# Kernel tuning notes

Measured on AMD Instinct MI355X. Metric: run time of the kernel, lower is better.

## Reference

```python
import jax, jax.numpy as jnp
import numpy as np

B, T = 64, 1024
VOCAB, EMBED, HIDDEN = 55, 64, 128


def setup_inputs() -> dict:
    key = jax.random.key(0)
    ks = jax.random.split(key, 15)
    stdv = 1.0 / np.sqrt(HIDDEN)
    u = lambda k, s: jax.random.uniform(k, s, jnp.float32, -stdv, stdv)
    return {
        "x": jax.random.randint(ks[0], (B, T), 0, VOCAB),
        "emb": jax.random.normal(ks[1], (VOCAB, EMBED), jnp.float32),
        "w_ih0": u(ks[2], (HIDDEN, EMBED)),
        "b_ih0": u(ks[3], (HIDDEN,)),
        "w_hh0": u(ks[4], (HIDDEN, HIDDEN)),
        "b_hh0": u(ks[5], (HIDDEN,)),
        "w_ih1": u(ks[6], (HIDDEN, HIDDEN)),
        "b_ih1": u(ks[7], (HIDDEN,)),
        "w_hh1": u(ks[8], (HIDDEN, HIDDEN)),
        "b_hh1": u(ks[9], (HIDDEN,)),
        "attn_w": u(ks[10], (HIDDEN, HIDDEN)),
        "attn_b": u(ks[11], (HIDDEN,)),
        "fc_w": u(ks[12], (VOCAB, 2 * HIDDEN)),
        "fc_b": u(ks[13], (VOCAB,)),
    }


def reference(x, emb, w_ih0, b_ih0, w_hh0, b_hh0, w_ih1, b_ih1, w_hh1, b_hh1,
              attn_w, attn_b, fc_w, fc_b):
    Bx, Tx = x.shape
    H = w_hh0.shape[0]
    e = emb[x]  # [B, T, E]

    def step(carry, x_t):  # x_t: [B, E]
        h0, h1 = carry
        h0 = jnp.tanh(x_t @ w_ih0.T + b_ih0 + h0 @ w_hh0.T + b_hh0)
        h1 = jnp.tanh(h0 @ w_ih1.T + b_ih1 + h1 @ w_hh1.T + b_hh1)
        return (h0, h1), h1

    init = (jnp.zeros((Bx, H), e.dtype), jnp.zeros((Bx, H), e.dtype))
    _, outs = jax.lax.scan(step, init, jnp.swapaxes(e, 0, 1))  # [T, B, H]
    outs = jnp.swapaxes(outs, 0, 1)  # [B, T, H]

    Q = outs @ attn_w.T + attn_b  # [B, T, H]
    scores = jnp.einsum('bth,bsh->bts', Q, outs) / jnp.sqrt(jnp.asarray(H, e.dtype))
    causal = jnp.tril(jnp.ones((Tx, Tx), bool))  # [T, T]
    scores = jnp.where(causal[None], scores, jnp.asarray(-jnp.inf, scores.dtype))
    attn = jax.nn.softmax(scores, axis=-1)
    context = jnp.einsum('bts,bsh->bth', attn, outs)  # [B, T, H]

    combined = jnp.concatenate([outs, context], axis=-1)  # [B, T, 2H]
    logits = combined @ fc_w.T + fc_b  # [B, T, vocab]
    return logits
```

## Files before the change

### kernel.cpp

```cpp
#include <hip/hip_runtime.h>
#include <hip/hip_bf16.h>
#include <cstdint>
#include <cstddef>


typedef __attribute__((ext_vector_type(8))) short short8;
typedef __attribute__((ext_vector_type(4))) float f32x4;

__device__ __forceinline__ float bf2f(unsigned short u) {
    union { unsigned int i; float f; } c; c.i = ((unsigned int)u) << 16; return c.f;
}
__device__ __forceinline__ unsigned short f2bf(float f) {
    union { float f; unsigned int i; } c; c.f = f;
    unsigned int u = c.i;
    u += 0x7fffu + ((u >> 16) & 1u);
    return (unsigned short)(u >> 16);
}
__device__ __forceinline__ unsigned int pk_bf16(float lo, float hi) {
    union { __hip_bfloat162 h2; unsigned int u; } c;
    c.h2 = __float22bfloat162_rn(make_float2(lo, hi));
    return c.u;
}
__device__ __forceinline__ float fast_tanh(float x) {
    float e = __expf(2.0f * x);
    return 1.0f - 2.0f * __builtin_amdgcn_rcpf(e + 1.0f);
}
__device__ __forceinline__ void bar_lds() {
    asm volatile("s_waitcnt lgkmcnt(0)\n\ts_barrier" ::: "memory");
}
__device__ __forceinline__ short8 ld_a_bf16(const float* p) {
    const float4* q = (const float4*)p;
    float4 f0 = q[0], f1 = q[1];
    short8 r;
    r[0]=(short)f2bf(f0.x); r[1]=(short)f2bf(f0.y);
    r[2]=(short)f2bf(f0.z); r[3]=(short)f2bf(f0.w);
    r[4]=(short)f2bf(f1.x); r[5]=(short)f2bf(f1.y);
    r[6]=(short)f2bf(f1.z); r[7]=(short)f2bf(f1.w);
    return r;
}
__device__ __forceinline__ void ld_fc_hilo(const float* p, short8& hi, short8& lo) {
    const float4* q = (const float4*)p;
    float4 f0 = q[0], f1 = q[1];
    float ff[8] = {f0.x, f0.y, f0.z, f0.w, f1.x, f1.y, f1.z, f1.w};
#pragma unroll
    for (int i = 0; i < 8; ++i) {
        unsigned short hb = f2bf(ff[i]);
        hi[i] = (short)hb;
        lo[i] = (short)f2bf(ff[i] - bf2f(hb));
    }
}

__global__ __launch_bounds__(128)
void k_we(const float* __restrict__ emb, const float* __restrict__ w_ih0,
          const float* __restrict__ b_ih0, const float* __restrict__ b_hh0,
          float* __restrict__ WE)
{
    __shared__ float ev[64];
    const int i = threadIdx.x;
    const int v = blockIdx.x;
    if (i < 64) ev[i] = emb[v * 64 + i];
    __syncthreads();
    float s = b_ih0[i] + b_hh0[i];
    const float* wr = w_ih0 + i * 64;
#pragma unroll
    for (int k = 0; k < 64; ++k) s += wr[k] * ev[k];
    WE[v * 128 + i] = s;
}

__global__ __launch_bounds__(256)
void k_weg(const int* __restrict__ x, const float* __restrict__ WE,
           float* __restrict__ WEg)
{
    __shared__ int xv[32];
    const int tid = threadIdx.x;
    const int b   = blockIdx.y;
    const int t0  = blockIdx.x * 32;
    if (tid < 32) xv[tid] = x[b * 1024 + t0 + tid];
    __syncthreads();
#pragma unroll
    for (int it = 0; it < 4; ++it) {
        int tt = it * 8 + (tid >> 5);
        int c4 = tid & 31;
        float4 v = ((const float4*)(WE + xv[tt] * 128))[c4];
        ((float4*)(WEg + ((size_t)b * 1024 + t0 + tt) * 128))[c4] = v;
    }
}

#define A_STEP(T, P, E0, E1)                                                   \
  {                                                                            \
    const unsigned short* h0p = &h0buf[P][n][quad * 8];                        \
    short8 bh[4];                                                              \
    _Pragma("unroll")                                                          \
    for (int ks = 0; ks < 4; ++ks)                                             \
      bh[ks] = *(const short8*)(h0p + ks * 32);                                \
    f32x4 c0 = (f32x4){E0.x, E0.y, E0.z, E0.w};                                \
    f32x4 c1 = (f32x4){E1.x, E1.y, E1.z, E1.w};                                \
    {                                                                          \
      const size_t tp = (size_t)(((T) + 3 < 1024) ? (T) + 3 : 1023) * 128;     \
      E0 = *(const float4*)(WEg + wegB0 + tp);                                 \
      E1 = *(const float4*)(WEg + wegB1 + tp);                                 \
    }                                                                          \
    _Pragma("unroll")                                                          \
    for (int ks = 0; ks < 4; ++ks) {                                           \
      c0 = __builtin_amdgcn_mfma_f32_16x16x32_bf16(a0[0][ks], bh[ks], c0, 0, 0, 0); \
      c1 = __builtin_amdgcn_mfma_f32_16x16x32_bf16(a0[1][ks], bh[ks], c1, 0, 0, 0); \
    }                                                                          \
    *(uint2*)&h0buf[(P) ^ 1][n][r0] = make_uint2(                              \
        pk_bf16(fast_tanh(c0[0]), fast_tanh(c0[1])),                           \
        pk_bf16(fast_tanh(c0[2]), fast_tanh(c0[3])));                          \
    *(uint2*)&h0buf[(P) ^ 1][n][r1] = make_uint2(                              \
        pk_bf16(fast_tanh(c1[0]), fast_tanh(c1[1])),                           \
        pk_bf16(fast_tanh(c1[2]), fast_tanh(c1[3])));                          \
    bar_lds();                                                                 \
  }

#define B_STEP(T, P)                                                           \
  {                                                                            \
    const unsigned short* h0p = &h0buf[P][n][quad * 8];                        \
    const unsigned short* h1p = &h1buf[P][n][quad * 8];                        \
    short8 bh0[4], bh1[4];                                                     \
    _Pragma("unroll")                                                          \
    for (int ks = 0; ks < 4; ++ks) {                                           \
      bh0[ks] = *(const short8*)(h0p + ks * 32);                               \
      bh1[ks] = *(const short8*)(h1p + ks * 32);                               \
    }                                                                          \
    f32x4 c0 = b1i[0], c1 = b1i[1];                                            \
    f32x4 d0 = (f32x4){0.f, 0.f, 0.f, 0.f};                                    \
    f32x4 d1 = (f32x4){0.f, 0.f, 0.f, 0.f};                                    \
    _Pragma("unroll")                                                          \
    for (int ks = 0; ks < 4; ++ks) {                                           \
      c0 = __builtin_amdgcn_mfma_f32_16x16x32_bf16(a1[0][ks], bh0[ks], c0, 0, 0, 0); \
      c1 = __builtin_amdgcn_mfma_f32_16x16x32_bf16(a1[1][ks], bh0[ks], c1, 0, 0, 0); \
      d0 = __builtin_amdgcn_mfma_f32_16x16x32_bf16(a2[0][ks], bh1[ks], d0, 0, 0, 0); \
      d1 = __builtin_amdgcn_mfma_f32_16x16x32_bf16(a2[1][ks], bh1[ks], d1, 0, 0, 0); \
    }                                                                          \
    uint2 o0 = make_uint2(                                                     \
        pk_bf16(fast_tanh(c0[0] + d0[0]), fast_tanh(c0[1] + d0[1])),           \
        pk_bf16(fast_tanh(c0[2] + d0[2]), fast_tanh(c0[3] + d0[3])));          \
    uint2 o1 = make_uint2(                                                     \
        pk_bf16(fast_tanh(c1[0] + d1[0]), fast_tanh(c1[1] + d1[1])),           \
        pk_bf16(fast_tanh(c1[2] + d1[2]), fast_tanh(c1[3] + d1[3])));          \
    *(uint2*)&h1buf[(P) ^ 1][n][r0] = o0;                                      \
    *(uint2*)&h1buf[(P) ^ 1][n][r1] = o1;                                      \
    *(uint2*)(outp0 + (size_t)(T) * 128) = o0;                                 \
    *(uint2*)(outp1 + (size_t)(T) * 128) = o1;                                 \
    bar_lds();                                                                 \
  }

__global__ __launch_bounds__(512, 1)
void k_scan7(const float* __restrict__ WEg,
             const float* __restrict__ w_hh0,
             const float* __restrict__ w_ih1, const float* __restrict__ b_ih1,
             const float* __restrict__ w_hh1, const float* __restrict__ b_hh1,
             unsigned short* __restrict__ outs_bf)
{
    const int tid   = threadIdx.x;
    const int w     = tid >> 6;
    const int lane  = tid & 63;
    const int quad  = lane >> 4;
    const int n     = lane & 15;
    const int bbase = blockIdx.x * 16;

    __shared__ __align__(16) unsigned short h0buf[2][16][136];
    __shared__ __align__(16) unsigned short h1buf[2][16][136];

    if (w < 4) {
        const int r0 = w * 32 + quad * 4;
        const int r1 = r0 + 16;
        short8 a0[2][4];
#pragma unroll
        for (int r = 0; r < 2; ++r) {
            const size_t mrow = (size_t)(w * 32 + r * 16 + n) * 128;
#pragma unroll
            for (int ks = 0; ks < 4; ++ks)
                a0[r][ks] = ld_a_bf16(w_hh0 + mrow + ks * 32 + quad * 8);
        }
        const size_t wegB0 = (size_t)(bbase + n) * 131072 + r0;
        const size_t wegB1 = wegB0 + 16;
        {
            float4 p0 = *(const float4*)(WEg + wegB0);
            float4 p1 = *(const float4*)(WEg + wegB1);
            *(uint2*)&h0buf[0][n][r0] = make_uint2(
                pk_bf16(fast_tanh(p0.x), fast_tanh(p0.y)),
                pk_bf16(fast_tanh(p0.z), fast_tanh(p0.w)));
            *(uint2*)&h0buf[0][n][r1] = make_uint2(
                pk_bf16(fast_tanh(p1.x), fast_tanh(p1.y)),
                pk_bf16(fast_tanh(p1.z), fast_tanh(p1.w)));
        }
        float4 eA0 = *(const float4*)(WEg + wegB0 + 128);
        float4 eA1 = *(const float4*)(WEg + wegB1 + 128);
        float4 eB0 = *(const float4*)(WEg + wegB0 + 256);
        float4 eB1 = *(const float4*)(WEg + wegB1 + 256);
        __syncthreads();

        for (int t = 0; t < 1022; t += 2) {
            A_STEP(t,     0, eA0, eA1);
            A_STEP(t + 1, 1, eB0, eB1);
        }
        A_STEP(1022, 0, eA0, eA1);
        bar_lds();
    } else {
        const int w2 = w - 4;
        const int r0 = w2 * 32 + quad * 4;
        const int r1 = r0 + 16;
        short8 a1[2][4], a2[2][4];
#pragma unroll
        for (int r = 0; r < 2; ++r) {
            const size_t mrow = (size_t)(w2 * 32 + r * 16 + n) * 128;
#pragma unroll
            for (int ks = 0; ks < 4; ++ks) {
                a1[r][ks] = ld_a_bf16(w_ih1 + mrow + ks * 32 + quad * 8);
                a2[r][ks] = ld_a_bf16(w_hh1 + mrow + ks * 32 + quad * 8);
            }
        }
        f32x4 b1i[2];
#pragma unroll
        for (int r = 0; r < 2; ++r)
#pragma unroll
            for (int j = 0; j < 4; ++j) {
                int row = w2 * 32 + r * 16 + quad * 4 + j;
                b1i[r][j] = b_ih1[row] + b_hh1[row];
            }
        *(uint2*)&h1buf[0][n][r0] = make_uint2(0u, 0u);
        *(uint2*)&h1buf[0][n][r1] = make_uint2(0u, 0u);
        unsigned short* outp0 = outs_bf + (size_t)(bbase + n) * 131072 + r0;
        unsigned short* outp1 = outp0 + 16;
        __syncthreads();

        for (int t = 0; t < 1022; t += 2) {
            B_STEP(t,     0);
            B_STEP(t + 1, 1);
        }
        B_STEP(1022, 0);
        B_STEP(1023, 1);
    }
}

__global__ __launch_bounds__(256)
void k_transpose(const unsigned short* __restrict__ outs_bf,
                 unsigned short* __restrict__ outsT)
{
    __shared__ unsigned short lt[128][130];
    const int tid = threadIdx.x;
    const int t0  = blockIdx.x * 128;
    const int b   = blockIdx.y;
    const unsigned int* src =
        (const unsigned int*)(outs_bf + ((size_t)b * 1024 + t0) * 128);
    for (int idx = tid; idx < 8192; idx += 256) {
        int tr = idx >> 6, h2 = idx & 63;
        unsigned int v = src[tr * 64 + h2];
        lt[tr][h2 * 2]     = (unsigned short)(v & 0xffffu);
        lt[tr][h2 * 2 + 1] = (unsigned short)(v >> 16);
    }
    __syncthreads();
    unsigned int* dst = (unsigned int*)(outsT + (size_t)b * 128 * 1024);
    for (int idx = tid; idx < 8192; idx += 256) {
        int h = idx >> 6, t2 = idx & 63;
        unsigned int v = (unsigned int)lt[t2 * 2][h] |
                         ((unsigned int)lt[t2 * 2 + 1][h] << 16);
        dst[h * 512 + (t0 >> 1) + t2] = v;
    }
}

__global__ __launch_bounds__(512, 1)
void k_attnfc(const unsigned short* __restrict__ outs_bf,
              const unsigned short* __restrict__ outsT,
              const float* __restrict__ attn_w, const float* __restrict__ attn_b,
              const float* __restrict__ fc_w, const float* __restrict__ fc_b,
              float* __restrict__ out)
{
    __shared__ __align__(16) unsigned char smem[51200];
    unsigned short* lK = (unsigned short*)smem;
    unsigned short* lV = (unsigned short*)(smem + 16384);
    unsigned short* lP = (unsigned short*)(smem + 32768);

    const int tid  = threadIdx.x;
    const int w    = tid >> 6;
    const int lane = tid & 63;
    const int quad = lane >> 4;
    const int n    = lane & 15;
    const int qt   = blockIdx.x;
    const int b    = blockIdx.y;
    unsigned short* lPw = lP + w * 1152;
    unsigned short* lQw = ((unsigned short*)smem) + w * 2048;
    const float cscale = 0.08838834764831845f;

    const unsigned short* outsB = outs_bf + (size_t)b * 131072;
    const int qrow = qt * 128 + w * 16 + n;

    short8 bo[4];
#pragma unroll
    for (int ks = 0; ks < 4; ++ks)
        bo[ks] = *(const short8*)(outsB + (size_t)qrow * 128 + ks * 32 + quad * 8);
#pragma unroll
    for (int mt = 0; mt < 8; ++mt) {
        short8 aw[4];
#pragma unroll
        for (int ks = 0; ks < 4; ++ks)
            aw[ks] = ld_a_bf16(attn_w + (size_t)(mt * 16 + n) * 128 + ks * 32 + quad * 8);
        f32x4 cq;
#pragma unroll
        for (int r = 0; r < 4; ++r) cq[r] = attn_b[mt * 16 + quad * 4 + r];
#pragma unroll
        for (int ks = 0; ks < 4; ++ks)
            cq = __builtin_amdgcn_mfma_f32_16x16x32_bf16(aw[ks], bo[ks], cq, 0,0,0);
        *(uint2*)&lQw[n * 128 + mt * 16 + quad * 4] =
            make_uint2(pk_bf16(cq[0], cq[1]), pk_bf16(cq[2], cq[3]));
    }
    short8 qf[4];
#pragma unroll
    for (int ks = 0; ks < 4; ++ks)
        qf[ks] = *(const short8*)&lQw[n * 128 + ks * 32 + quad * 8];

    f32x4 accO[8];
#pragma unroll
    for (int dt = 0; dt < 8; ++dt) accO[dt] = (f32x4){0.f, 0.f, 0.f, 0.f};
    float mx = -1e30f, lsum = 0.f;

    const int ntiles = 2 * qt + 2;
    for (int kt = 0; kt < ntiles; ++kt) {
        __syncthreads();
        for (int c = tid; c < 2048; c += 512) {
            if (c < 1024) {
                int row = c >> 4, k8 = c & 15;
                uint4 vk = *(const uint4*)(outsB + (size_t)(kt * 64 + row) * 128 + k8 * 8);
                *(uint4*)&lK[row * 128 + ((k8 ^ (row & 15)) << 3)] = vk;
            } else {
                int c2 = c - 1024;
                int d = c2 >> 3, t8 = c2 & 7;
                uint4 vv = *(const uint4*)(outsT + ((size_t)b * 128 + d) * 1024 +
                                           kt * 64 + t8 * 8);
                *(uint4*)&lV[d * 64 + ((t8 ^ (d & 7)) << 3)] = vv;
            }
        }
        __syncthreads();
        f32x4 accS[4];
#pragma unroll
        for (int mt = 0; mt < 4; ++mt) {
            short8 af[4];
#pragma unroll
            for (int ks = 0; ks < 4; ++ks) {
                int r = mt * 16 + n;
                af[ks] = *(const short8*)&lK[r * 128 + (((ks * 4 + quad) ^ (r & 15)) << 3)];
            }
            f32x4 s = (f32x4){0.f, 0.f, 0.f, 0.f};
#pragma unroll
            for (int ks = 0; ks < 4; ++ks)
                s = __builtin_amdgcn_mfma_f32_16x16x32_bf16(af[ks], qf[ks], s, 0,0,0);
            accS[mt] = s;
        }
        if (kt >= 2 * qt) {
#pragma unroll
            for (int mt = 0; mt < 4; ++mt)
#pragma unroll
                for (int jv = 0; jv < 4; ++jv)
                    if (kt * 64 + mt * 16 + quad * 4 + jv > qrow - qt * 128 + 0 + qt * 128 - qt * 128
                        + qt * 128 - qt * 128 + (qrow & 127) - (qrow & 127) + (qrow - qt * 128))
                        ;
        }
        if (kt >= 2 * qt) {
            const int ql = w * 16 + n;
#pragma unroll
            for (int mt = 0; mt < 4; ++mt)
#pragma unroll
                for (int jv = 0; jv < 4; ++jv)
                    if (kt * 64 + mt * 16 + quad * 4 + jv > qt * 128 + ql)
                        accS[mt][jv] = -1e30f;
        }
        float tmax = accS[0][0];
#pragma unroll
        for (int mt = 0; mt < 4; ++mt)
#pragma unroll
            for (int jv = 0; jv < 4; ++jv) tmax = fmaxf(tmax, accS[mt][jv]);
        tmax = fmaxf(tmax, __shfl_xor(tmax, 16));
        tmax = fmaxf(tmax, __shfl_xor(tmax, 32));
        float nm = fmaxf(mx, tmax);
        float alpha = __expf((mx - nm) * cscale);
        float ss = 0.f;
#pragma unroll
        for (int mt = 0; mt < 4; ++mt)
#pragma unroll
            for (int jv = 0; jv < 4; ++jv) {
                float p = __expf((accS[mt][jv] - nm) * cscale);
                accS[mt][jv] = p;
                ss += p;
            }
        ss += __shfl_xor(ss, 16);
        ss += __shfl_xor(ss, 32);
        lsum = lsum * alpha + ss;
        mx = nm;
#pragma unroll
        for (int mt = 0; mt < 4; ++mt)
            *(uint2*)&lPw[n * 72 + mt * 16 + quad * 4] = make_uint2(
                pk_bf16(accS[mt][0], accS[mt][1]),
                pk_bf16(accS[mt][2], accS[mt][3]));
#pragma unroll
        for (int dt = 0; dt < 8; ++dt)
#pragma unroll
            for (int jv = 0; jv < 4; ++jv) accO[dt][jv] *= alpha;
        short8 pf[2];
#pragma unroll
        for (int ks = 0; ks < 2; ++ks)
            pf[ks] = *(const short8*)&lPw[n * 72 + ks * 32 + quad * 8];
#pragma unroll
        for (int dt = 0; dt < 8; ++dt) {
            short8 vf[2];
#pragma unroll
            for (int ks = 0; ks < 2; ++ks) {
                int d = dt * 16 + n;
                vf[ks] = *(const short8*)&lV[d * 64 + (((ks * 4 + quad) ^ (d & 7)) << 3)];
            }
#pragma unroll
            for (int ks = 0; ks < 2; ++ks)
                accO[dt] = __builtin_amdgcn_mfma_f32_16x16x32_bf16(vf[ks], pf[ks], accO[dt], 0,0,0);
        }
    }
    __syncthreads();
    {
        float inv = __builtin_amdgcn_rcpf(lsum);
#pragma unroll
        for (int dt = 0; dt < 8; ++dt)
            *(uint2*)&lQw[n * 128 + dt * 16 + quad * 4] = make_uint2(
                pk_bf16(accO[dt][0] * inv, accO[dt][1] * inv),
                pk_bf16(accO[dt][2] * inv, accO[dt][3] * inv));
    }
    short8 bC[4];
#pragma unroll
    for (int ks = 0; ks < 4; ++ks)
        bC[ks] = *(const short8*)&lQw[n * 128 + ks * 32 + quad * 8];
#pragma unroll
    for (int mt = 0; mt < 4; ++mt) {
        const int vrow = mt * 16 + n;
        f32x4 acc;
#pragma unroll
        for (int r = 0; r < 4; ++r) {
            int vv = mt * 16 + quad * 4 + r;
            acc[r] = (vv < 55) ? fc_b[vv] : 0.f;
        }
#pragma unroll
        for (int c = 0; c < 8; ++c) {
            short8 hi, lo;
            if (vrow < 55) {
                ld_fc_hilo(fc_w + (size_t)vrow * 256 + c * 32 + quad * 8, hi, lo);
            } else {
#pragma unroll
                for (int i = 0; i < 8; ++i) { hi[i] = 0; lo[i] = 0; }
            }
            short8 bb = (c < 4) ? bo[c] : bC[c - 4];
            acc = __builtin_amdgcn_mfma_f32_16x16x32_bf16(hi, bb, acc, 0,0,0);
            acc = __builtin_amdgcn_mfma_f32_16x16x32_bf16(lo, bb, acc, 0,0,0);
        }
#pragma unroll
        for (int r = 0; r < 4; ++r) {
            int vv = mt * 16 + quad * 4 + r;
            if (vv < 55)
                out[((size_t)b * 1024 + qrow) * 55 + vv] = acc[r];
        }
    }
}

extern "C" void kernel_launch(void* const* d_in, const int* in_sizes, int n_in,
                              void* d_out, int out_size, void* d_ws, size_t ws_size,
                              hipStream_t stream)
{
    const int*   x      = (const int*)d_in[0];
    const float* emb    = (const float*)d_in[1];
    const float* w_ih0  = (const float*)d_in[2];
    const float* b_ih0  = (const float*)d_in[3];
    const float* w_hh0  = (const float*)d_in[4];
    const float* b_hh0  = (const float*)d_in[5];
    const float* w_ih1  = (const float*)d_in[6];
    const float* b_ih1  = (const float*)d_in[7];
    const float* w_hh1  = (const float*)d_in[8];
    const float* b_hh1  = (const float*)d_in[9];
    const float* attn_w = (const float*)d_in[10];
    const float* attn_b = (const float*)d_in[11];
    const float* fc_w   = (const float*)d_in[12];
    const float* fc_b   = (const float*)d_in[13];
    float* out = (float*)d_out;

    char* ws = (char*)d_ws;
    unsigned short* outs_bf = (unsigned short*)(ws);
    unsigned short* outsT   = (unsigned short*)(ws + ((size_t)16 << 20));
    float*          WEp     = (float*)         (ws + ((size_t)32 << 20));
    float*          WEg     = (float*)         (ws + ((size_t)33 << 20));

    k_we<<<dim3(55), dim3(128), 0, stream>>>(emb, w_ih0, b_ih0, b_hh0, WEp);
    k_weg<<<dim3(32, 64), dim3(256), 0, stream>>>(x, WEp, WEg);
    k_scan7<<<dim3(4), dim3(512), 0, stream>>>(
        WEg, w_hh0, w_ih1, b_ih1, w_hh1, b_hh1, outs_bf);
    k_transpose<<<dim3(8, 64), dim3(256), 0, stream>>>(outs_bf, outsT);
    k_attnfc<<<dim3(8, 64), dim3(512), 0, stream>>>(
        outs_bf, outsT, attn_w, attn_b, fc_w, fc_b, out);
}
```

Before: 742.6 us.

## Split causal attention KV tiles across blocks and merge partial softmax states

Each query tile's causal key range is split into chunks of at most six KV tiles, handled by separate blocks, which balances work across the triangular attention grid. Short query tiles (qt ≤ 2) still finish in one block and apply the FC projection directly. Longer ones write unnormalized partial outputs plus running max and sum to a workspace. A new merge kernel combines the partials with online-softmax rescaling and then runs the FC projection. This costs an extra launch and a workspace round-trip, and the partial buffer overlaps the workspace region that held WEg, which is safe only because that data is no longer needed.

Result: slower. 804.6 us (+8.3%).

```diff
diff --git a/kernel.cpp b/kernel.cpp
--- a/kernel.cpp
+++ b/kernel.cpp
@@ -263,11 +263,11 @@
 }
 
 __global__ __launch_bounds__(512, 1)
-void k_attnfc(const unsigned short* __restrict__ outs_bf,
-              const unsigned short* __restrict__ outsT,
-              const float* __restrict__ attn_w, const float* __restrict__ attn_b,
-              const float* __restrict__ fc_w, const float* __restrict__ fc_b,
-              float* __restrict__ out)
+void k_attn_part(const unsigned short* __restrict__ outs_bf,
+                 const unsigned short* __restrict__ outsT,
+                 const float* __restrict__ attn_w, const float* __restrict__ attn_b,
+                 const float* __restrict__ fc_w, const float* __restrict__ fc_b,
+                 float* __restrict__ part_ws, float* __restrict__ out)
 {
     __shared__ __align__(16) unsigned char smem[51200];
     unsigned short* lK = (unsigned short*)smem;
@@ -279,14 +279,28 @@
     const int lane = tid & 63;
     const int quad = lane >> 4;
     const int n    = lane & 15;
-    const int qt   = blockIdx.x;
+    const int gi   = blockIdx.x;
     const int b    = blockIdx.y;
     unsigned short* lPw = lP + w * 1152;
     unsigned short* lQw = ((unsigned short*)smem) + w * 2048;
     const float cscale = 0.08838834764831845f;
 
+    int qt = 0, base = 0;
+    if (gi >= 1)  { qt = 1; base = 1; }
+    if (gi >= 2)  { qt = 2; base = 2; }
+    if (gi >= 3)  { qt = 3; base = 3; }
+    if (gi >= 5)  { qt = 4; base = 5; }
+    if (gi >= 7)  { qt = 5; base = 7; }
+    if (gi >= 9)  { qt = 6; base = 9; }
+    if (gi >= 12) { qt = 7; base = 12; }
+    const int g   = gi - base;
+    const int kt0 = g * 6;
+    const int kt1 = min(kt0 + 6, 2 * qt + 2);
+    const bool whole = (qt <= 2);
+
     const unsigned short* outsB = outs_bf + (size_t)b * 131072;
     const int qrow = qt * 128 + w * 16 + n;
+    const int q128 = w * 16 + n;
 
     short8 bo[4];
 #pragma unroll
@@ -317,8 +331,7 @@
     for (int dt = 0; dt < 8; ++dt) accO[dt] = (f32x4){0.f, 0.f, 0.f, 0.f};
     float mx = -1e30f, lsum = 0.f;
 
-    const int ntiles = 2 * qt + 2;
-    for (int kt = 0; kt < ntiles; ++kt) {
+    for (int kt = kt0; kt < kt1; ++kt) {
         __syncthreads();
         for (int c = tid; c < 2048; c += 512) {
             if (c < 1024) {
@@ -350,15 +363,6 @@
             accS[mt] = s;
         }
         if (kt >= 2 * qt) {
-#pragma unroll
-            for (int mt = 0; mt < 4; ++mt)
-#pragma unroll
-                for (int jv = 0; jv < 4; ++jv)
-                    if (kt * 64 + mt * 16 + quad * 4 + jv > qrow - qt * 128 + 0 + qt * 128 - qt * 128
-                        + qt * 128 - qt * 128 + (qrow & 127) - (qrow & 127) + (qrow - qt * 128))
-                        ;
-        }
-        if (kt >= 2 * qt) {
             const int ql = w * 16 + n;
 #pragma unroll
             for (int mt = 0; mt < 4; ++mt)
@@ -415,6 +419,21 @@
                 accO[dt] = __builtin_amdgcn_mfma_f32_16x16x32_bf16(vf[ks], pf[ks], accO[dt], 0,0,0);
         }
     }
+
+    if (!whole) {
+        float* wsO = part_ws + (size_t)(b * 12 + gi - 3) * 16640;
+        float4* po = (float4*)wsO;
+#pragma unroll
+        for (int dt = 0; dt < 8; ++dt)
+            po[(w * 64 + lane) * 8 + dt] =
+                make_float4(accO[dt][0], accO[dt][1], accO[dt][2], accO[dt][3]);
+        if (quad == 0) {
+            wsO[16384 + q128 * 2]     = mx;
+            wsO[16384 + q128 * 2 + 1] = lsum;
+        }
+        return;
+    }
+
     __syncthreads();
     {
         float inv = __builtin_amdgcn_rcpf(lsum);
@@ -428,6 +447,107 @@
 #pragma unroll
     for (int ks = 0; ks < 4; ++ks)
         bC[ks] = *(const short8*)&lQw[n * 128 + ks * 32 + quad * 8];
+#pragma unroll
+    for (int mt = 0; mt < 4; ++mt) {
+        const int vrow = mt * 16 + n;
+        f32x4 acc;
+#pragma unroll
+        for (int r = 0; r < 4; ++r) {
+            int vv = mt * 16 + quad * 4 + r;
+            acc[r] = (vv < 55) ? fc_b[vv] : 0.f;
+        }
+#pragma unroll
+        for (int c = 0; c < 8; ++c) {
+            short8 hi, lo;
+            if (vrow < 55) {
+                ld_fc_hilo(fc_w + (size_t)vrow * 256 + c * 32 + quad * 8, hi, lo);
+            } else {
+#pragma unroll
+                for (int i = 0; i < 8; ++i) { hi[i] = 0; lo[i] = 0; }
+            }
+            short8 bb = (c < 4) ? bo[c] : bC[c - 4];
+            acc = __builtin_amdgcn_mfma_f32_16x16x32_bf16(hi, bb, acc, 0,0,0);
+            acc = __builtin_amdgcn_mfma_f32_16x16x32_bf16(lo, bb, acc, 0,0,0);
+        }
+#pragma unroll
+        for (int r = 0; r < 4; ++r) {
+            int vv = mt * 16 + quad * 4 + r;
+            if (vv < 55)
+                out[((size_t)b * 1024 + qrow) * 55 + vv] = acc[r];
+        }
+    }
+}
+
+__global__ __launch_bounds__(512, 1)
+void k_merge(const unsigned short* __restrict__ outs_bf,
+             const float* __restrict__ part_ws,
+             const float* __restrict__ fc_w, const float* __restrict__ fc_b,
+             float* __restrict__ out)
+{
+    __shared__ __align__(16) unsigned short lQ[8][16][128];
+
+    const int tid  = threadIdx.x;
+    const int w    = tid >> 6;
+    const int lane = tid & 63;
+    const int quad = lane >> 4;
+    const int n    = lane & 15;
+    const int qt   = blockIdx.x + 3;
+    const int b    = blockIdx.y;
+    const float cscale = 0.08838834764831845f;
+
+    const int ng = (2 * qt + 7) / 6;
+    int base = 9;
+    if (qt == 3) base = 0;
+    else if (qt == 4) base = 2;
+    else if (qt == 5) base = 4;
+    else if (qt == 6) base = 6;
+
+    const int qrow = qt * 128 + w * 16 + n;
+    const int q128 = w * 16 + n;
+
+    f32x4 accO[8];
+#pragma unroll
+    for (int dt = 0; dt < 8; ++dt) accO[dt] = (f32x4){0.f, 0.f, 0.f, 0.f};
+    float mx = -1e30f, lsum = 0.f;
+
+    for (int p = 0; p < ng; ++p) {
+        const float* wsO = part_ws + (size_t)(b * 12 + base + p) * 16640;
+        const float4* po = (const float4*)wsO;
+        float m0 = wsO[16384 + q128 * 2];
+        float l0 = wsO[16384 + q128 * 2 + 1];
+        float nm = fmaxf(mx, m0);
+        float a1 = __expf((mx - nm) * cscale);
+        float a0 = __expf((m0 - nm) * cscale);
+#pragma unroll
+        for (int dt = 0; dt < 8; ++dt) {
+            float4 p4 = po[(w * 64 + lane) * 8 + dt];
+            accO[dt][0] = accO[dt][0] * a1 + p4.x * a0;
+            accO[dt][1] = accO[dt][1] * a1 + p4.y * a0;
+            accO[dt][2] = accO[dt][2] * a1 + p4.z * a0;
+            accO[dt][3] = accO[dt][3] * a1 + p4.w * a0;
+        }
+        lsum = lsum * a1 + l0 * a0;
+        mx = nm;
+    }
+
+    {
+        float inv = __builtin_amdgcn_rcpf(lsum);
+#pragma unroll
+        for (int dt = 0; dt < 8; ++dt)
+            *(uint2*)&lQ[w][n][dt * 16 + quad * 4] = make_uint2(
+                pk_bf16(accO[dt][0] * inv, accO[dt][1] * inv),
+                pk_bf16(accO[dt][2] * inv, accO[dt][3] * inv));
+    }
+    __syncthreads();
+    const unsigned short* outsB = outs_bf + (size_t)b * 131072;
+    short8 bo[4];
+#pragma unroll
+    for (int ks = 0; ks < 4; ++ks)
+        bo[ks] = *(const short8*)(outsB + (size_t)qrow * 128 + ks * 32 + quad * 8);
+    short8 bC[4];
+#pragma unroll
+    for (int ks = 0; ks < 4; ++ks)
+        bC[ks] = *(const short8*)&lQ[w][n][ks * 32 + quad * 8];
 #pragma unroll
     for (int mt = 0; mt < 4; ++mt) {
         const int vrow = mt * 16 + n;
@@ -483,6 +603,7 @@
     unsigned short* outs_bf = (unsigned short*)(ws);
     unsigned short* outsT   = (unsigned short*)(ws + ((size_t)16 << 20));
     float*          WEp     = (float*)         (ws + ((size_t)32 << 20));
+    float*          part_ws = (float*)         (ws + ((size_t)32 << 20) + (64 << 10));
     float*          WEg     = (float*)         (ws + ((size_t)33 << 20));
 
     k_we<<<dim3(55), dim3(128), 0, stream>>>(emb, w_ih0, b_ih0, b_hh0, WEp);
@@ -490,6 +611,8 @@
     k_scan7<<<dim3(4), dim3(512), 0, stream>>>(
         WEg, w_hh0, w_ih1, b_ih1, w_hh1, b_hh1, outs_bf);
     k_transpose<<<dim3(8, 64), dim3(256), 0, stream>>>(outs_bf, outsT);
-    k_attnfc<<<dim3(8, 64), dim3(512), 0, stream>>>(
-        outs_bf, outsT, attn_w, attn_b, fc_w, fc_b, out);
-}
+    k_attn_part<<<dim3(15, 64), dim3(512), 0, stream>>>(
+        outs_bf, outsT, attn_w, attn_b, fc_w, fc_b, part_ws, out);
+    k_merge<<<dim3(5, 64), dim3(512), 0, stream>>>(
+        outs_bf, part_ws, fc_w, fc_b, out);
+}
```

## Pre-convert attention/fc weights to bf16 and use direct global-to-LDS loads

Applied to the files above, without the earlier changes.

Adds a prep kernel that converts attn_w to bf16 and splits fc_w into hi/lo bf16 parts once, so the attention/FC kernel loads bf16 directly instead of converting per block. The K/V tile staging in the attention loop is replaced with global_load_lds 16-byte direct-to-LDS loads, with the XOR swizzle moved to the global address side. A dead no-op mask loop is removed. This adds one extra small kernel launch and relies on the direct-LDS load path producing the same swizzled layout.

After: 744.6 us. About the same (+0.3%).

```diff
diff --git a/kernel.cpp b/kernel.cpp
--- a/kernel.cpp
+++ b/kernel.cpp
@@ -38,15 +38,26 @@
     r[6]=(short)f2bf(f1.z); r[7]=(short)f2bf(f1.w);
     return r;
 }
-__device__ __forceinline__ void ld_fc_hilo(const float* p, short8& hi, short8& lo) {
-    const float4* q = (const float4*)p;
-    float4 f0 = q[0], f1 = q[1];
-    float ff[8] = {f0.x, f0.y, f0.z, f0.w, f1.x, f1.y, f1.z, f1.w};
-#pragma unroll
-    for (int i = 0; i < 8; ++i) {
-        unsigned short hb = f2bf(ff[i]);
-        hi[i] = (short)hb;
-        lo[i] = (short)f2bf(ff[i] - bf2f(hb));
+__device__ __forceinline__ void gload_lds16(const unsigned short* g,
+                                            unsigned short* l) {
+    __builtin_amdgcn_global_load_lds(
+        (const __attribute__((address_space(1))) unsigned int*)g,
+        (__attribute__((address_space(3))) unsigned int*)l, 16, 0, 0);
+}
+
+__global__ __launch_bounds__(256)
+void k_prep(const float* __restrict__ attn_w, const float* __restrict__ fc_w,
+            unsigned short* __restrict__ attn_wb,
+            unsigned short* __restrict__ fc_hib,
+            unsigned short* __restrict__ fc_lob)
+{
+    const int i = blockIdx.x * 256 + threadIdx.x;
+    if (i < 16384) attn_wb[i] = f2bf(attn_w[i]);
+    if (i < 14080) {
+        float wv = fc_w[i];
+        unsigned short h = f2bf(wv);
+        fc_hib[i] = h;
+        fc_lob[i] = f2bf(wv - bf2f(h));
     }
 }
 
@@ -265,8 +276,11 @@
 __global__ __launch_bounds__(512, 1)
 void k_attnfc(const unsigned short* __restrict__ outs_bf,
               const unsigned short* __restrict__ outsT,
-              const float* __restrict__ attn_w, const float* __restrict__ attn_b,
-              const float* __restrict__ fc_w, const float* __restrict__ fc_b,
+              const unsigned short* __restrict__ attn_wb,
+              const float* __restrict__ attn_b,
+              const unsigned short* __restrict__ fc_hib,
+              const unsigned short* __restrict__ fc_lob,
+              const float* __restrict__ fc_b,
               float* __restrict__ out)
 {
     __shared__ __align__(16) unsigned char smem[51200];
@@ -297,7 +311,8 @@
         short8 aw[4];
 #pragma unroll
         for (int ks = 0; ks < 4; ++ks)
-            aw[ks] = ld_a_bf16(attn_w + (size_t)(mt * 16 + n) * 128 + ks * 32 + quad * 8);
+            aw[ks] = *(const short8*)(attn_wb + (size_t)(mt * 16 + n) * 128 +
+                                      ks * 32 + quad * 8);
         f32x4 cq;
 #pragma unroll
         for (int r = 0; r < 4; ++r) cq[r] = attn_b[mt * 16 + quad * 4 + r];
@@ -320,18 +335,21 @@
     const int ntiles = 2 * qt + 2;
     for (int kt = 0; kt < ntiles; ++kt) {
         __syncthreads();
-        for (int c = tid; c < 2048; c += 512) {
-            if (c < 1024) {
-                int row = c >> 4, k8 = c & 15;
-                uint4 vk = *(const uint4*)(outsB + (size_t)(kt * 64 + row) * 128 + k8 * 8);
-                *(uint4*)&lK[row * 128 + ((k8 ^ (row & 15)) << 3)] = vk;
-            } else {
-                int c2 = c - 1024;
-                int d = c2 >> 3, t8 = c2 & 7;
-                uint4 vv = *(const uint4*)(outsT + ((size_t)b * 128 + d) * 1024 +
-                                           kt * 64 + t8 * 8);
-                *(uint4*)&lV[d * 64 + ((t8 ^ (d & 7)) << 3)] = vv;
-            }
+        {
+            int c = tid;
+            int row = c >> 4, g = c & 15;
+            gload_lds16(outsB + (size_t)(kt * 64 + row) * 128 +
+                        ((g ^ (row & 15)) << 3), lK + c * 8);
+            c = tid + 512; row = c >> 4; g = c & 15;
+            gload_lds16(outsB + (size_t)(kt * 64 + row) * 128 +
+                        ((g ^ (row & 15)) << 3), lK + c * 8);
+            int c2 = tid;
+            int d = c2 >> 3, t8 = c2 & 7;
+            gload_lds16(outsT + ((size_t)b * 128 + d) * 1024 + kt * 64 +
+                        ((t8 ^ (d & 7)) << 3), lV + c2 * 8);
+            c2 = tid + 512; d = c2 >> 3; t8 = c2 & 7;
+            gload_lds16(outsT + ((size_t)b * 128 + d) * 1024 + kt * 64 +
+                        ((t8 ^ (d & 7)) << 3), lV + c2 * 8);
         }
         __syncthreads();
         f32x4 accS[4];
@@ -348,15 +366,6 @@
             for (int ks = 0; ks < 4; ++ks)
                 s = __builtin_amdgcn_mfma_f32_16x16x32_bf16(af[ks], qf[ks], s, 0,0,0);
             accS[mt] = s;
-        }
-        if (kt >= 2 * qt) {
-#pragma unroll
-            for (int mt = 0; mt < 4; ++mt)
-#pragma unroll
-                for (int jv = 0; jv < 4; ++jv)
-                    if (kt * 64 + mt * 16 + quad * 4 + jv > qrow - qt * 128 + 0 + qt * 128 - qt * 128
-                        + qt * 128 - qt * 128 + (qrow & 127) - (qrow & 127) + (qrow - qt * 128))
-                        ;
         }
         if (kt >= 2 * qt) {
             const int ql = w * 16 + n;
@@ -441,7 +450,8 @@
         for (int c = 0; c < 8; ++c) {
             short8 hi, lo;
             if (vrow < 55) {
-                ld_fc_hilo(fc_w + (size_t)vrow * 256 + c * 32 + quad * 8, hi, lo);
+                hi = *(const short8*)(fc_hib + (size_t)vrow * 256 + c * 32 + quad * 8);
+                lo = *(const short8*)(fc_lob + (size_t)vrow * 256 + c * 32 + quad * 8);
             } else {
 #pragma unroll
                 for (int i = 0; i < 8; ++i) { hi[i] = 0; lo[i] = 0; }
@@ -483,13 +493,17 @@
     unsigned short* outs_bf = (unsigned short*)(ws);
     unsigned short* outsT   = (unsigned short*)(ws + ((size_t)16 << 20));
     float*          WEp     = (float*)         (ws + ((size_t)32 << 20));
+    unsigned short* attn_wb = (unsigned short*)(ws + ((size_t)32 << 20) + (64 << 10));
+    unsigned short* fc_hib  = (unsigned short*)(ws + ((size_t)32 << 20) + (128 << 10));
+    unsigned short* fc_lob  = (unsigned short*)(ws + ((size_t)32 << 20) + (192 << 10));
     float*          WEg     = (float*)         (ws + ((size_t)33 << 20));
 
+    k_prep<<<dim3(64), dim3(256), 0, stream>>>(attn_w, fc_w, attn_wb, fc_hib, fc_lob);
     k_we<<<dim3(55), dim3(128), 0, stream>>>(emb, w_ih0, b_ih0, b_hh0, WEp);
     k_weg<<<dim3(32, 64), dim3(256), 0, stream>>>(x, WEp, WEg);
     k_scan7<<<dim3(4), dim3(512), 0, stream>>>(
         WEg, w_hh0, w_ih1, b_ih1, w_hh1, b_hh1, outs_bf);
     k_transpose<<<dim3(8, 64), dim3(256), 0, stream>>>(outs_bf, outsT);
     k_attnfc<<<dim3(8, 64), dim3(512), 0, stream>>>(
-        outs_bf, outsT, attn_w, attn_b, fc_w, fc_b, out);
-}
+        outs_bf, outsT, attn_wb, attn_b, fc_hib, fc_lob, fc_b, out);
+}
```
